# Optimization experiments

Hardware: AMD Instinct MI355X
Metric: run time of the kernel (lower is better)

## Reference

```python
import jax, jax.numpy as jnp
import numpy as np

HIDDEN = 1024
N_HEAD = 16
D_HEAD = HIDDEN // N_HEAD


def setup_inputs() -> dict:
    key = jax.random.key(0)
    ks = jax.random.split(key, 12)
    B, S, H = 2, 2048, HIDDEN
    scale = 1.0 / np.sqrt(H)
    inp = {
        "q": jax.random.normal(ks[0], (B, S, H), jnp.float32),
        "k": jax.random.normal(ks[1], (B, S, H), jnp.float32),
        "v": jax.random.normal(ks[2], (B, S, H), jnp.float32),
        "mask": jnp.ones((B, 1, S, S), jnp.int32),
        "w_q": jax.random.normal(ks[3], (H, H), jnp.float32) * scale,
        "b_q": jnp.zeros((H,), jnp.float32),
        "w_k": jax.random.normal(ks[4], (H, H), jnp.float32) * scale,
        "b_k": jnp.zeros((H,), jnp.float32),
        "w_v": jax.random.normal(ks[5], (H, H), jnp.float32) * scale,
        "b_v": jnp.zeros((H,), jnp.float32),
        "w_o": jax.random.normal(ks[6], (H, H), jnp.float32) * scale,
        "b_o": jnp.zeros((H,), jnp.float32),
    }
    return inp


def reference(q, k, v, mask, w_q, b_q, w_k, b_k, w_v, b_v, w_o, b_o):
    B, Sq, H = q.shape
    Sk = k.shape[1]
    # projections (weights stored as [in, out])
    qh = (q @ w_q + b_q).reshape(B, Sq, N_HEAD, D_HEAD).transpose(0, 2, 1, 3)
    kh = (k @ w_k + b_k).reshape(B, Sk, N_HEAD, D_HEAD).transpose(0, 2, 1, 3)
    vh = (v @ w_v + b_v).reshape(B, Sk, N_HEAD, D_HEAD).transpose(0, 2, 1, 3)
    scores = jnp.einsum("bhqd,bhkd->bhqk", qh, kh) * (D_HEAD ** -0.5)
    scores = jnp.where(mask == 0, jnp.float32(-10000.0), scores)
    attn = jax.nn.softmax(scores, axis=-1)
    out = jnp.einsum("bhqk,bhkd->bhqd", attn, vh)
    out = out.transpose(0, 2, 1, 3).reshape(B, Sq, H)
    return out @ w_o + b_o
```

## Files before the change

### kernel.cpp

```cpp
#include <hip/hip_runtime.h>
#include <hip/hip_bf16.h>
#include <stdint.h>

#define S_LEN 2048
#define HID   1024
#define NHEAD 16
#define DHEAD 64
#define BATCH 2

#define QSCALE 0.18033688f
#define MASKNEG -14427.0f

typedef __bf16 bf16_t;
typedef __bf16 bf16x4 __attribute__((ext_vector_type(4)));
typedef __bf16 bf16x8 __attribute__((ext_vector_type(8)));
typedef float  f32x4  __attribute__((ext_vector_type(4)));


__device__ __forceinline__ void gl_lds16(const bf16_t* g, bf16_t* l) {
  __builtin_amdgcn_global_load_lds((const __attribute__((address_space(1))) void*)g,
                                   (__attribute__((address_space(3))) void*)l,
                                   16, 0, 0);
}

template<int TR, int TC>
__device__ __forceinline__ void stage_tile(const bf16_t* __restrict__ g, int ldg,
                                           bf16_t* lds, int wave, int lane) {
  constexpr int CH = TC / 8;
  constexpr int NINST = (TR * CH) / 64;
  #pragma unroll
  for (int i = wave; i < NINST; i += 4) {
    int slot = i * 64 + lane;
    int r  = slot / CH;
    int cs = slot & (CH - 1);
    int c  = cs ^ (r & (CH - 1));
    gl_lds16(g + (size_t)r * ldg + c * 8, lds + i * 512);
  }
}

template<int CH>
__device__ __forceinline__ bf16x8 frag_ld(const bf16_t* lds, int row, int kchunk) {
  int cs = kchunk ^ (row & (CH - 1));
  return *(const bf16x8*)(lds + (row * CH + cs) * 8);
}

__global__ __launch_bounds__(256) void cvt3(const float* __restrict__ q,
                                            const float* __restrict__ k,
                                            const float* __restrict__ v,
                                            bf16_t* __restrict__ qb,
                                            bf16_t* __restrict__ kb,
                                            bf16_t* __restrict__ vb) {
  int which = blockIdx.y;
  const float* src = which == 0 ? q : which == 1 ? k : v;
  bf16_t* dst = which == 0 ? qb : which == 1 ? kb : vb;
  size_t i = ((size_t)blockIdx.x * 256 + threadIdx.x) * 4;
  float4 u = *(const float4*)(src + i);
  bf16x4 o = {(bf16_t)u.x, (bf16_t)u.y, (bf16_t)u.z, (bf16_t)u.w};
  *(bf16x4*)(dst + i) = o;
}

__global__ __launch_bounds__(256) void transpose_w4(
    const float* __restrict__ w0, const float* __restrict__ w1,
    const float* __restrict__ w2, const float* __restrict__ w3,
    bf16_t* __restrict__ wt, int* __restrict__ flags) {
  if (blockIdx.x == 0 && blockIdx.y == 0 && blockIdx.z == 0) {
    flags[threadIdx.x] = -1;
    flags[threadIdx.x + 256] = -1;
  }
  __shared__ float t[64][65];
  const float* W = blockIdx.z == 0 ? w0 : blockIdx.z == 1 ? w1 : blockIdx.z == 2 ? w2 : w3;
  bf16_t* WT = wt + (size_t)blockIdx.z * HID * HID;
  int tx = threadIdx.x & 63, ty = threadIdx.x >> 6;
  int r0 = blockIdx.y * 64, c0 = blockIdx.x * 64;
  #pragma unroll
  for (int i = ty; i < 64; i += 4) t[i][tx] = W[(size_t)(r0 + i) * HID + c0 + tx];
  __syncthreads();
  #pragma unroll
  for (int i = ty; i < 64; i += 4) WT[(size_t)(c0 + i) * HID + r0 + tx] = (bf16_t)t[tx][i];
}

__global__ __launch_bounds__(256) void mask_flags(const int* __restrict__ mask,
                                                  int* __restrict__ flags) {
  int qtile = blockIdx.x, rg = blockIdx.y, b = blockIdx.z;
  const int* base = mask + (size_t)b * S_LEN * S_LEN
                  + (size_t)(qtile * 128 + rg * 16) * S_LEN;
  int tid = threadIdx.x;
  int kt = tid >> 4;
  int ok = 1;
  #pragma unroll
  for (int r = 0; r < 16; ++r) {
    const int4* p = (const int4*)(base + (size_t)r * S_LEN + tid * 8);
    int4 a = p[0], c = p[1];
    ok &= (a.x != 0) & (a.y != 0) & (a.z != 0) & (a.w != 0) &
          (c.x != 0) & (c.y != 0) & (c.z != 0) & (c.w != 0);
  }
  __shared__ int oks[16];
  if (tid < 16) oks[tid] = -1;
  __syncthreads();
  if (!ok) atomicAnd(&oks[kt], 0);
  __syncthreads();
  if (tid < 16 && oks[tid] == 0) atomicAnd(&flags[(b * 16 + qtile) * 16 + tid], 0);
}

__global__ __launch_bounds__(256) void qkv_gemm(
    const bf16_t* __restrict__ qb, const bf16_t* __restrict__ kb, const bf16_t* __restrict__ vb,
    const bf16_t* __restrict__ wT,
    const float* __restrict__ bq, const float* __restrict__ bk, const float* __restrict__ bv,
    bf16_t* __restrict__ Qh, bf16_t* __restrict__ Kh, bf16_t* __restrict__ VhT) {
  int mode = blockIdx.z;
  const bf16_t* A    = mode == 0 ? qb : mode == 1 ? kb : vb;
  const bf16_t* Bt   = wT + (size_t)mode * HID * HID;
  const float*  bias = mode == 0 ? bq : mode == 1 ? bk : bv;

  __shared__ __align__(16) bf16_t As[128 * 64];
  __shared__ __align__(16) bf16_t Bs[128 * 64];

  int tid = threadIdx.x, wave = tid >> 6, lane = tid & 63;
  int lane15 = lane & 15, quad = lane >> 4;
  int m0 = blockIdx.x * 128, n0 = blockIdx.y * 128;
  int wm = (wave >> 1) * 64, wn = (wave & 1) * 64;

  f32x4 zero4 = {0.f, 0.f, 0.f, 0.f};
  f32x4 acc[4][4];
  #pragma unroll
  for (int t = 0; t < 4; ++t)
    #pragma unroll
    for (int n = 0; n < 4; ++n) acc[t][n] = zero4;

  for (int k0 = 0; k0 < HID; k0 += 64) {
    stage_tile<128, 64>(A  + (size_t)m0 * HID + k0, HID, As, wave, lane);
    stage_tile<128, 64>(Bt + (size_t)n0 * HID + k0, HID, Bs, wave, lane);
    __syncthreads();
    #pragma unroll
    for (int kc = 0; kc < 2; ++kc) {
      bf16x8 af[4], bfr[4];
      #pragma unroll
      for (int t = 0; t < 4; ++t) af[t]  = frag_ld<8>(As, wm + t * 16 + lane15, kc * 4 + quad);
      #pragma unroll
      for (int n = 0; n < 4; ++n) bfr[n] = frag_ld<8>(Bs, wn + n * 16 + lane15, kc * 4 + quad);
      if (mode < 2) {
        #pragma unroll
        for (int t = 0; t < 4; ++t)
          #pragma unroll
          for (int n = 0; n < 4; ++n)
            acc[t][n] = __builtin_amdgcn_mfma_f32_16x16x32_bf16(af[t], bfr[n], acc[t][n], 0, 0, 0);
      } else {
        #pragma unroll
        for (int t = 0; t < 4; ++t)
          #pragma unroll
          for (int n = 0; n < 4; ++n)
            acc[t][n] = __builtin_amdgcn_mfma_f32_16x16x32_bf16(bfr[n], af[t], acc[t][n], 0, 0, 0);
      }
    }
    __syncthreads();
  }

  if (mode < 2) {
    float sc = (mode == 0) ? QSCALE : 1.0f;
    bf16_t* dst = (mode == 0 ? Qh : Kh);
    #pragma unroll
    for (int t = 0; t < 4; ++t) {
      #pragma unroll
      for (int n = 0; n < 4; ++n) {
        int col = n0 + wn + n * 16 + lane15;
        float bb = bias[col];
        #pragma unroll
        for (int i = 0; i < 4; ++i) {
          int row = m0 + wm + t * 16 + quad * 4 + i;
          bf16_t o = (bf16_t)((acc[t][n][i] + bb) * sc);
          int b = row >> 11, s = row & 2047;
          int h = col >> 6,  d = col & 63;
          dst[((size_t)(b * NHEAD + h) * S_LEN + s) * DHEAD + d] = o;
        }
      }
    }
  } else {
    #pragma unroll
    for (int n = 0; n < 4; ++n) {
      int dbase = n0 + wn + n * 16 + quad * 4;
      float4 bb4 = *(const float4*)(bias + dbase);
      #pragma unroll
      for (int t = 0; t < 4; ++t) {
        int token = m0 + wm + t * 16 + lane15;
        int b = token >> 11, s = token & 2047;
        #pragma unroll
        for (int i = 0; i < 4; ++i) {
          int dg = dbase + i;
          int h = dg >> 6, d = dg & 63;
          float bb = i == 0 ? bb4.x : i == 1 ? bb4.y : i == 2 ? bb4.z : bb4.w;
          VhT[((size_t)(b * NHEAD + h) * DHEAD + d) * S_LEN + s] = (bf16_t)(acc[t][n][i] + bb);
        }
      }
    }
  }
}

__global__ __launch_bounds__(256) void attn_kernel(
    const bf16_t* __restrict__ Qh, const bf16_t* __restrict__ Kh, const bf16_t* __restrict__ VhT,
    const int* __restrict__ mask, const int* __restrict__ flags,
    bf16_t* __restrict__ O) {
  __shared__ __align__(16) bf16_t Ks[128 * 64];
  __shared__ __align__(16) bf16_t VTs[80 * 128];
  __shared__ __align__(16) bf16_t Ps[128 * 128];

  int tid = threadIdx.x, wave = tid >> 6, lane = tid & 63;
  int lane15 = lane & 15, quad = lane >> 4;
  int bh = blockIdx.y, b = bh >> 4, h = bh & 15;
  int qt = blockIdx.x;
  int wrow = wave * 32;

  if (tid < 128) VTs[64 * 128 + tid] = (bf16_t)1.0f;

  stage_tile<128, 64>(Qh + ((size_t)bh * S_LEN + qt * 128) * DHEAD, DHEAD, Ps, wave, lane);
  __syncthreads();
  bf16x8 qa[2][2];
  #pragma unroll
  for (int kc = 0; kc < 2; ++kc)
    #pragma unroll
    for (int nq = 0; nq < 2; ++nq)
      qa[kc][nq] = frag_ld<8>(Ps, wrow + nq * 16 + lane15, kc * 4 + quad);

  f32x4 zero4 = {0.f, 0.f, 0.f, 0.f};
  f32x4 o_acc[2][5];
  #pragma unroll
  for (int nq = 0; nq < 2; ++nq)
    #pragma unroll
    for (int mt = 0; mt < 5; ++mt) o_acc[nq][mt] = zero4;

  for (int kt = 0; kt < S_LEN / 128; ++kt) {
    stage_tile<128, 64>(Kh + ((size_t)bh * S_LEN + kt * 128) * DHEAD, DHEAD, Ks, wave, lane);
    stage_tile<64, 128>(VhT + (size_t)bh * DHEAD * S_LEN + kt * 128, S_LEN, VTs, wave, lane);
    __syncthreads();

    f32x4 sa[2][8];
    #pragma unroll
    for (int nq = 0; nq < 2; ++nq)
      #pragma unroll
      for (int mc = 0; mc < 8; ++mc) sa[nq][mc] = zero4;
    #pragma unroll
    for (int kc = 0; kc < 2; ++kc) {
      bf16x8 kf[8];
      #pragma unroll
      for (int mc = 0; mc < 8; ++mc) kf[mc] = frag_ld<8>(Ks, mc * 16 + lane15, kc * 4 + quad);
      #pragma unroll
      for (int nq = 0; nq < 2; ++nq)
        #pragma unroll
        for (int mc = 0; mc < 8; ++mc)
          sa[nq][mc] = __builtin_amdgcn_mfma_f32_16x16x32_bf16(kf[mc], qa[kc][nq], sa[nq][mc], 0, 0, 0);
    }

    if (flags[(b * 16 + qt) * 16 + kt] == 0) {
      #pragma unroll
      for (int nq = 0; nq < 2; ++nq)
        #pragma unroll
        for (int mc = 0; mc < 8; ++mc)
          #pragma unroll
          for (int i = 0; i < 4; ++i) {
            int q = qt * 128 + wrow + nq * 16 + lane15;
            int c = kt * 128 + mc * 16 + quad * 4 + i;
            if (mask[(size_t)b * S_LEN * S_LEN + (size_t)q * S_LEN + c] == 0)
              sa[nq][mc][i] = MASKNEG;
          }
    }

    #pragma unroll
    for (int nq = 0; nq < 2; ++nq) {
      int q = wrow + nq * 16 + lane15;
      #pragma unroll
      for (int mc = 0; mc < 8; ++mc) {
        bf16x4 pk = {(bf16_t)exp2f(sa[nq][mc][0]), (bf16_t)exp2f(sa[nq][mc][1]),
                     (bf16_t)exp2f(sa[nq][mc][2]), (bf16_t)exp2f(sa[nq][mc][3])};
        int chunk = mc * 2 + (quad >> 1);
        int slot = chunk ^ (q & 15);
        *(bf16x4*)(Ps + q * 128 + slot * 8 + (quad & 1) * 4) = pk;
      }
    }

    #pragma unroll
    for (int kc = 0; kc < 4; ++kc) {
      bf16x8 vf[5], pf[2];
      #pragma unroll
      for (int mt = 0; mt < 5; ++mt) vf[mt] = frag_ld<16>(VTs, mt * 16 + lane15, kc * 4 + quad);
      #pragma unroll
      for (int nq = 0; nq < 2; ++nq) pf[nq] = frag_ld<16>(Ps, wrow + nq * 16 + lane15, kc * 4 + quad);
      #pragma unroll
      for (int nq = 0; nq < 2; ++nq)
        #pragma unroll
        for (int mt = 0; mt < 5; ++mt)
          o_acc[nq][mt] = __builtin_amdgcn_mfma_f32_16x16x32_bf16(vf[mt], pf[nq], o_acc[nq][mt], 0, 0, 0);
    }
    __syncthreads();
  }

  #pragma unroll
  for (int nq = 0; nq < 2; ++nq) {
    float lval = __shfl(o_acc[nq][4][0], lane15);
    float inv = 1.0f / lval;
    int s = qt * 128 + wrow + nq * 16 + lane15;
    size_t orow = ((size_t)b * S_LEN + s) * HID + h * DHEAD;
    #pragma unroll
    for (int mt = 0; mt < 4; ++mt) {
      bf16x4 ov = {(bf16_t)(o_acc[nq][mt][0] * inv), (bf16_t)(o_acc[nq][mt][1] * inv),
                   (bf16_t)(o_acc[nq][mt][2] * inv), (bf16_t)(o_acc[nq][mt][3] * inv)};
      *(bf16x4*)(O + orow + mt * 16 + quad * 4) = ov;
    }
  }
}

__global__ __launch_bounds__(256) void oproj_gemm(
    const bf16_t* __restrict__ A, const bf16_t* __restrict__ Bt,
    const float* __restrict__ bias, float* __restrict__ out) {
  __shared__ __align__(16) bf16_t As[128 * 64];
  __shared__ __align__(16) bf16_t Bs[128 * 64];

  int tid = threadIdx.x, wave = tid >> 6, lane = tid & 63;
  int lane15 = lane & 15, quad = lane >> 4;
  int m0 = blockIdx.x * 128, n0 = blockIdx.y * 128;
  int wm = (wave >> 1) * 64, wn = (wave & 1) * 64;

  f32x4 zero4 = {0.f, 0.f, 0.f, 0.f};
  f32x4 acc[4][4];
  #pragma unroll
  for (int t = 0; t < 4; ++t)
    #pragma unroll
    for (int n = 0; n < 4; ++n) acc[t][n] = zero4;

  for (int k0 = 0; k0 < HID; k0 += 64) {
    stage_tile<128, 64>(A  + (size_t)m0 * HID + k0, HID, As, wave, lane);
    stage_tile<128, 64>(Bt + (size_t)n0 * HID + k0, HID, Bs, wave, lane);
    __syncthreads();
    #pragma unroll
    for (int kc = 0; kc < 2; ++kc) {
      bf16x8 af[4], bfr[4];
      #pragma unroll
      for (int t = 0; t < 4; ++t) af[t]  = frag_ld<8>(As, wm + t * 16 + lane15, kc * 4 + quad);
      #pragma unroll
      for (int n = 0; n < 4; ++n) bfr[n] = frag_ld<8>(Bs, wn + n * 16 + lane15, kc * 4 + quad);
      #pragma unroll
      for (int t = 0; t < 4; ++t)
        #pragma unroll
        for (int n = 0; n < 4; ++n)
          acc[t][n] = __builtin_amdgcn_mfma_f32_16x16x32_bf16(af[t], bfr[n], acc[t][n], 0, 0, 0);
    }
    __syncthreads();
  }

  #pragma unroll
  for (int t = 0; t < 4; ++t) {
    #pragma unroll
    for (int n = 0; n < 4; ++n) {
      int col = n0 + wn + n * 16 + lane15;
      float bb = bias[col];
      #pragma unroll
      for (int i = 0; i < 4; ++i) {
        int row = m0 + wm + t * 16 + quad * 4 + i;
        out[(size_t)row * HID + col] = acc[t][n][i] + bb;
      }
    }
  }
}

extern "C" void kernel_launch(void* const* d_in, const int* in_sizes, int n_in,
                              void* d_out, int out_size, void* d_ws, size_t ws_size,
                              hipStream_t stream) {
  (void)in_sizes; (void)n_in; (void)out_size; (void)ws_size;
  const float* q  = (const float*)d_in[0];
  const float* k  = (const float*)d_in[1];
  const float* v  = (const float*)d_in[2];
  const int*  mask = (const int*)d_in[3];
  const float* wq = (const float*)d_in[4];
  const float* bq = (const float*)d_in[5];
  const float* wk = (const float*)d_in[6];
  const float* bk = (const float*)d_in[7];
  const float* wv = (const float*)d_in[8];
  const float* bv = (const float*)d_in[9];
  const float* wo = (const float*)d_in[10];
  const float* bo = (const float*)d_in[11];

  char* ws = (char*)d_ws;
  bf16_t* wT    = (bf16_t*)(ws);
  bf16_t* Qh    = (bf16_t*)(ws + (8u  << 20));
  bf16_t* Kh    = (bf16_t*)(ws + (16u << 20));
  bf16_t* VhT   = (bf16_t*)(ws + (24u << 20));
  bf16_t* qb    = (bf16_t*)(ws + (32u << 20));
  bf16_t* kb    = (bf16_t*)(ws + (40u << 20));
  bf16_t* vb    = (bf16_t*)(ws + (48u << 20));
  int* flags    = (int*)(ws + (56u << 20));
  bf16_t* Obuf  = qb;

  cvt3<<<dim3(4096, 3), 256, 0, stream>>>(q, k, v, qb, kb, vb);
  transpose_w4<<<dim3(16, 16, 4), 256, 0, stream>>>(wq, wk, wv, wo, wT, flags);
  mask_flags<<<dim3(16, 8, 2), 256, 0, stream>>>(mask, flags);
  qkv_gemm<<<dim3(32, 8, 3), 256, 0, stream>>>(qb, kb, vb, wT, bq, bk, bv, Qh, Kh, VhT);
  attn_kernel<<<dim3(16, 32), 256, 0, stream>>>(Qh, Kh, VhT, mask, flags, Obuf);
  oproj_gemm<<<dim3(32, 8), 256, 0, stream>>>(Obuf, wT + (size_t)3 * HID * HID, bo, (float*)d_out);
}
```

Measured before the change: 275.2 us.

## Double-buffer K/V tiles in attention with 64-key steps and MFMA priority

The attention loop now works on 64-key tiles with two LDS buffers for K and V^T. Loads for the next tile are issued before the current tile's QK^T, softmax and PV work, so global-to-LDS traffic can overlap with compute. s_setprio is raised around the MFMA bursts to favour matrix issue. In exchange the loop runs twice as many iterations with a barrier each, and each iteration has less work over which to hide latency.

```diff
diff --git a/kernel.cpp b/kernel.cpp
--- a/kernel.cpp
+++ b/kernel.cpp
@@ -199,9 +199,9 @@
     const bf16_t* __restrict__ Qh, const bf16_t* __restrict__ Kh, const bf16_t* __restrict__ VhT,
     const int* __restrict__ mask, const int* __restrict__ flags,
     bf16_t* __restrict__ O) {
-  __shared__ __align__(16) bf16_t Ks[128 * 64];
-  __shared__ __align__(16) bf16_t VTs[80 * 128];
-  __shared__ __align__(16) bf16_t Ps[128 * 128];
+  __shared__ __align__(16) bf16_t Ks[2][64 * 64];
+  __shared__ __align__(16) bf16_t VTs[2][80 * 64];
+  __shared__ __align__(16) bf16_t Ps[128 * 64];
 
   int tid = threadIdx.x, wave = tid >> 6, lane = tid & 63;
   int lane15 = lane & 15, quad = lane >> 4;
@@ -209,10 +209,20 @@
   int qt = blockIdx.x;
   int wrow = wave * 32;
 
-  if (tid < 128) VTs[64 * 128 + tid] = (bf16_t)1.0f;
+  const bf16_t* Kbase = Kh + (size_t)bh * S_LEN * DHEAD;
+  const bf16_t* Vbase = VhT + (size_t)bh * DHEAD * S_LEN;
+  const int* flagrow = flags + (b * 16 + qt) * 16;
+
+  if (tid < 64) {
+    VTs[0][64 * 64 + tid] = (bf16_t)1.0f;
+    VTs[1][64 * 64 + tid] = (bf16_t)1.0f;
+  }
 
   stage_tile<128, 64>(Qh + ((size_t)bh * S_LEN + qt * 128) * DHEAD, DHEAD, Ps, wave, lane);
+  stage_tile<64, 64>(Kbase, DHEAD, Ks[0], wave, lane);
+  stage_tile<64, 64>(Vbase, S_LEN, VTs[0], wave, lane);
   __syncthreads();
+
   bf16x8 qa[2][2];
   #pragma unroll
   for (int kc = 0; kc < 2; ++kc)
@@ -227,37 +237,47 @@
     #pragma unroll
     for (int mt = 0; mt < 5; ++mt) o_acc[nq][mt] = zero4;
 
-  for (int kt = 0; kt < S_LEN / 128; ++kt) {
-    stage_tile<128, 64>(Kh + ((size_t)bh * S_LEN + kt * 128) * DHEAD, DHEAD, Ks, wave, lane);
-    stage_tile<64, 128>(VhT + (size_t)bh * DHEAD * S_LEN + kt * 128, S_LEN, VTs, wave, lane);
-    __syncthreads();
-
-    f32x4 sa[2][8];
-    #pragma unroll
-    for (int nq = 0; nq < 2; ++nq)
-      #pragma unroll
-      for (int mc = 0; mc < 8; ++mc) sa[nq][mc] = zero4;
-    #pragma unroll
-    for (int kc = 0; kc < 2; ++kc) {
-      bf16x8 kf[8];
-      #pragma unroll
-      for (int mc = 0; mc < 8; ++mc) kf[mc] = frag_ld<8>(Ks, mc * 16 + lane15, kc * 4 + quad);
+  int cur = 0;
+  for (int kt = 0; kt < S_LEN / 64; ++kt) {
+    if (kt + 1 < S_LEN / 64) {
+      stage_tile<64, 64>(Kbase + (size_t)(kt + 1) * 64 * DHEAD, DHEAD, Ks[cur ^ 1], wave, lane);
+      stage_tile<64, 64>(Vbase + (kt + 1) * 64, S_LEN, VTs[cur ^ 1], wave, lane);
+    }
+    const bf16_t* Kc = Ks[cur];
+    const bf16_t* Vc = VTs[cur];
+
+    f32x4 sa[2][4];
+    {
+      bf16x8 kf[4];
+      #pragma unroll
+      for (int mc = 0; mc < 4; ++mc) kf[mc] = frag_ld<8>(Kc, mc * 16 + lane15, quad);
+      __builtin_amdgcn_s_setprio(1);
       #pragma unroll
       for (int nq = 0; nq < 2; ++nq)
         #pragma unroll
-        for (int mc = 0; mc < 8; ++mc)
-          sa[nq][mc] = __builtin_amdgcn_mfma_f32_16x16x32_bf16(kf[mc], qa[kc][nq], sa[nq][mc], 0, 0, 0);
-    }
-
-    if (flags[(b * 16 + qt) * 16 + kt] == 0) {
+        for (int mc = 0; mc < 4; ++mc)
+          sa[nq][mc] = __builtin_amdgcn_mfma_f32_16x16x32_bf16(kf[mc], qa[0][nq], zero4, 0, 0, 0);
+      __builtin_amdgcn_s_setprio(0);
+      #pragma unroll
+      for (int mc = 0; mc < 4; ++mc) kf[mc] = frag_ld<8>(Kc, mc * 16 + lane15, 4 + quad);
+      __builtin_amdgcn_s_setprio(1);
       #pragma unroll
       for (int nq = 0; nq < 2; ++nq)
         #pragma unroll
-        for (int mc = 0; mc < 8; ++mc)
+        for (int mc = 0; mc < 4; ++mc)
+          sa[nq][mc] = __builtin_amdgcn_mfma_f32_16x16x32_bf16(kf[mc], qa[1][nq], sa[nq][mc], 0, 0, 0);
+      __builtin_amdgcn_s_setprio(0);
+    }
+
+    if (flagrow[kt >> 1] == 0) {
+      #pragma unroll
+      for (int nq = 0; nq < 2; ++nq)
+        #pragma unroll
+        for (int mc = 0; mc < 4; ++mc)
           #pragma unroll
           for (int i = 0; i < 4; ++i) {
             int q = qt * 128 + wrow + nq * 16 + lane15;
-            int c = kt * 128 + mc * 16 + quad * 4 + i;
+            int c = kt * 64 + mc * 16 + quad * 4 + i;
             if (mask[(size_t)b * S_LEN * S_LEN + (size_t)q * S_LEN + c] == 0)
               sa[nq][mc][i] = MASKNEG;
           }
@@ -267,29 +287,33 @@
     for (int nq = 0; nq < 2; ++nq) {
       int q = wrow + nq * 16 + lane15;
       #pragma unroll
-      for (int mc = 0; mc < 8; ++mc) {
+      for (int mc = 0; mc < 4; ++mc) {
         bf16x4 pk = {(bf16_t)exp2f(sa[nq][mc][0]), (bf16_t)exp2f(sa[nq][mc][1]),
                      (bf16_t)exp2f(sa[nq][mc][2]), (bf16_t)exp2f(sa[nq][mc][3])};
         int chunk = mc * 2 + (quad >> 1);
-        int slot = chunk ^ (q & 15);
-        *(bf16x4*)(Ps + q * 128 + slot * 8 + (quad & 1) * 4) = pk;
+        int slot = chunk ^ (q & 7);
+        *(bf16x4*)(Ps + q * 64 + slot * 8 + (quad & 1) * 4) = pk;
       }
     }
 
     #pragma unroll
-    for (int kc = 0; kc < 4; ++kc) {
+    for (int kc = 0; kc < 2; ++kc) {
       bf16x8 vf[5], pf[2];
       #pragma unroll
-      for (int mt = 0; mt < 5; ++mt) vf[mt] = frag_ld<16>(VTs, mt * 16 + lane15, kc * 4 + quad);
-      #pragma unroll
-      for (int nq = 0; nq < 2; ++nq) pf[nq] = frag_ld<16>(Ps, wrow + nq * 16 + lane15, kc * 4 + quad);
+      for (int mt = 0; mt < 5; ++mt) vf[mt] = frag_ld<8>(Vc, mt * 16 + lane15, kc * 4 + quad);
+      #pragma unroll
+      for (int nq = 0; nq < 2; ++nq) pf[nq] = frag_ld<8>(Ps, wrow + nq * 16 + lane15, kc * 4 + quad);
+      __builtin_amdgcn_s_setprio(1);
       #pragma unroll
       for (int nq = 0; nq < 2; ++nq)
         #pragma unroll
         for (int mt = 0; mt < 5; ++mt)
           o_acc[nq][mt] = __builtin_amdgcn_mfma_f32_16x16x32_bf16(vf[mt], pf[nq], o_acc[nq][mt], 0, 0, 0);
-    }
+      __builtin_amdgcn_s_setprio(0);
+    }
+
     __syncthreads();
+    cur ^= 1;
   }
 
   #pragma unroll
```

Result: no change. 279.3 us (+1.5%).
